# Performance work log

Hardware: AMD Instinct MI355X
Metric: run time of the kernel (lower is better)

The kernel has to match this reference:

```python
import jax, jax.numpy as jnp
import numpy as np

N_GENE = 4762
N_CELL = 847


def _graph_conv(x_src, src, dst, n_src, n_dst, W, b):
    """DGL GraphConv with norm='both': D_src^{-1/2} A D_dst^{-1/2} X W + b."""
    ones_e = jnp.ones(src.shape, jnp.float32)
    deg_out = jax.ops.segment_sum(ones_e, src, num_segments=n_src)
    norm_src = jnp.clip(deg_out, 1.0, None) ** -0.5
    feat = x_src * norm_src[:, None]            # [n_src, d]
    msg = feat[src]                              # gather  [E, d]
    agg = jax.ops.segment_sum(msg, dst, num_segments=n_dst)  # scatter-add [n_dst, d]
    deg_in = jax.ops.segment_sum(ones_e, dst, num_segments=n_dst)
    norm_dst = jnp.clip(deg_in, 1.0, None) ** -0.5
    return (agg * norm_dst[:, None]) @ W + b


def setup_inputs() -> dict:
    key = jax.random.key(0)
    ks = jax.random.split(key, 12)
    E = 200000
    d = 256
    inp = {
        "gene_emb": jax.random.normal(ks[0], (N_GENE, d), jnp.float32),
        "cell_emb": jax.random.normal(ks[1], (N_CELL, d), jnp.float32),
        "W_g2c": jax.random.normal(ks[2], (d, d), jnp.float32) * (1.0 / np.sqrt(d)),
        "b_g2c": jnp.zeros((d,), jnp.float32),
        "W_c2g": jax.random.normal(ks[3], (d, d), jnp.float32) * (1.0 / np.sqrt(d)),
        "b_c2g": jnp.zeros((d,), jnp.float32),
        "Wp": jax.random.normal(ks[4], (2 * d, 1), jnp.float32) * (1.0 / np.sqrt(2 * d)),
        "bp": jnp.zeros((1,), jnp.float32),
        "g2c_src": jax.random.randint(ks[5], (E,), 0, N_GENE, jnp.int32),
        "g2c_dst": jax.random.randint(ks[6], (E,), 0, N_CELL, jnp.int32),
        "c2g_src": jax.random.randint(ks[7], (E,), 0, N_CELL, jnp.int32),
        "c2g_dst": jax.random.randint(ks[8], (E,), 0, N_GENE, jnp.int32),
        "dec_src": jax.random.randint(ks[9], (E,), 0, N_GENE, jnp.int32),
        "dec_dst": jax.random.randint(ks[10], (E,), 0, N_CELL, jnp.int32),
    }
    return inp


def reference(gene_emb, cell_emb, W_g2c, b_g2c, W_c2g, b_c2g, Wp, bp,
              g2c_src, g2c_dst, c2g_src, c2g_dst, dec_src, dec_dst):
    # HeteroGraphConv (aggregate='sum'): each dst type receives from one relation here.
    h_cell = _graph_conv(gene_emb, g2c_src, g2c_dst, N_GENE, N_CELL, W_g2c, b_g2c)
    h_gene = _graph_conv(cell_emb, c2g_src, c2g_dst, N_CELL, N_GENE, W_c2g, b_c2g)
    h_gene = jax.nn.relu(h_gene)
    h_cell = jax.nn.relu(h_cell)
    # HeteroMLPPredictor: concat(src_h, dst_h) @ Wp + bp on dec_graph edges.
    x = jnp.concatenate([h_gene[dec_src], h_cell[dec_dst]], axis=1)  # [E_dec, 512]
    score = x @ Wp + bp                                               # [E_dec, 1]
    return (score, h_gene, h_cell)
```

## Files before the change

kernel.cpp:

```cpp
#include <hip/hip_runtime.h>

#define N_GENE 4762
#define N_CELL 847
#define NEDGE  200000
#define D      256
#define NPART  64

typedef __attribute__((ext_vector_type(8))) short short8;
typedef __attribute__((ext_vector_type(4))) float f32x4;

#define S_G_OUT 0
#define S_C_IN  (S_G_OUT + N_GENE)
#define S_C_OUT (S_C_IN + N_CELL)
#define S_G_IN  (S_C_OUT + N_CELL)
#define NBINS   (S_G_IN + N_GENE)

#define ALIGN8(x) (((x) + 7) & ~7)

#define A_DEG      0
#define A_NRM      (A_DEG + NBINS)
#define A_OFFS_C   (A_NRM + NBINS)
#define A_OFFS_G   (A_OFFS_C + N_CELL + 1)
#define A_SORT_C   ALIGN8(A_OFFS_G + N_GENE + 1)
#define A_SORT_G   (A_SORT_C + 2 * NEDGE)
#define A_PART     (A_SORT_G + 2 * NEDGE)
#define A_SG       (A_PART + NPART * NBINS)
#define A_SC       (A_SG + N_GENE)
#define A_GENE_BF  ALIGN8(A_SC + N_CELL)
#define A_CELL_BF  ALIGN8(A_GENE_BF + N_GENE * D / 2)
#define A_WT1_BF   ALIGN8(A_CELL_BF + N_CELL * D / 2)
#define A_WT2_BF   ALIGN8(A_WT1_BF + D * D / 2)
#define A_AGGC_BF  ALIGN8(A_WT2_BF + D * D / 2)
#define A_AGGG_BF  ALIGN8(A_AGGC_BF + N_CELL * D / 2)

__device__ __forceinline__ unsigned short f2bf(float f) {
    unsigned u = __float_as_uint(f);
    u = (u + 0x7FFFu + ((u >> 16) & 1u)) >> 16;
    return (unsigned short)u;
}
__device__ __forceinline__ float bf2f(unsigned short b) {
    return __uint_as_float(((unsigned)b) << 16);
}

__global__ __launch_bounds__(1024) void k_pre(
        const int* __restrict__ g2c_src, const int* __restrict__ g2c_dst,
        const int* __restrict__ c2g_src, const int* __restrict__ c2g_dst,
        const float* __restrict__ gene_emb, const float* __restrict__ cell_emb,
        const float* __restrict__ W_g2c, const float* __restrict__ W_c2g,
        int* __restrict__ partial,
        unsigned short* __restrict__ gene_bf, unsigned short* __restrict__ cell_bf,
        unsigned short* __restrict__ wt1, unsigned short* __restrict__ wt2) {
    __shared__ int sh[NBINS];
    int B = blockIdx.x, T = threadIdx.x;
    if (B < NPART) {
        for (int j = T; j < NBINS; j += 1024) sh[j] = 0;
        __syncthreads();
        const int chunk = (NEDGE + NPART - 1) / NPART;
        int e0 = B * chunk, e1 = min(NEDGE, e0 + chunk);
        for (int e = e0 + T; e < e1; e += 1024) {
            atomicAdd(&sh[S_G_OUT + g2c_src[e]], 1);
            atomicAdd(&sh[S_C_IN  + g2c_dst[e]], 1);
            atomicAdd(&sh[S_C_OUT + c2g_src[e]], 1);
            atomicAdd(&sh[S_G_IN  + c2g_dst[e]], 1);
        }
        __syncthreads();
        int* pp = partial + B * NBINS;
        for (int j = T; j < NBINS; j += 1024) pp[j] = sh[j];
    } else {
        const int NG = N_GENE * D, NC = N_CELL * D, NW = D * D;
        const int total = NG + NC + 2 * NW;
        for (int i = (B - NPART) * 1024 + T; i < total; i += NPART * 1024) {
            if (i < NG) {
                gene_bf[i] = f2bf(gene_emb[i]);
            } else if (i < NG + NC) {
                int j = i - NG;
                cell_bf[j] = f2bf(cell_emb[j]);
            } else if (i < NG + NC + NW) {
                int j = i - NG - NC;
                wt1[j] = f2bf(W_g2c[(j & 255) * D + (j >> 8)]);
            } else {
                int j = i - NG - NC - NW;
                wt2[j] = f2bf(W_c2g[(j & 255) * D + (j >> 8)]);
            }
        }
    }
}

__global__ void k_reduce(int* __restrict__ partial, int* __restrict__ deg,
                         float* __restrict__ nrm) {
    int j = blockIdx.x * blockDim.x + threadIdx.x;
    if (j < NBINS) {
        int s = 0;
        #pragma unroll
        for (int b0 = 0; b0 < NPART; b0 += 32) {
            int t[32];
            #pragma unroll
            for (int u = 0; u < 32; u++) t[u] = partial[(b0 + u) * NBINS + j];
            #pragma unroll
            for (int u = 0; u < 32; u++) { partial[(b0 + u) * NBINS + j] = s; s += t[u]; }
        }
        deg[j] = s;
        nrm[j] = rsqrtf(fmaxf((float)s, 1.0f));
    }
}

__global__ __launch_bounds__(1024) void k_scatter(
        const int* __restrict__ g2c_src, const int* __restrict__ g2c_dst,
        const int* __restrict__ c2g_src, const int* __restrict__ c2g_dst,
        const int* __restrict__ deg, const int* __restrict__ partial,
        const float* __restrict__ nrm,
        int* __restrict__ offsC, int* __restrict__ offsG,
        int2* __restrict__ sortC, int2* __restrict__ sortG) {
    __shared__ int soffs[N_GENE + 1];
    __shared__ int scur[N_GENE];
    __shared__ int wsum[16];
    int T = threadIdx.x, blk = blockIdx.x, dir = blockIdx.y;
    const int* src  = dir ? c2g_src : g2c_src;
    const int* dst  = dir ? c2g_dst : g2c_dst;
    const int* dgs  = dir ? deg + S_G_IN : deg + S_C_IN;
    const float* nsv = dir ? nrm + S_C_OUT : nrm + S_G_OUT;
    int seg         = dir ? S_G_IN : S_C_IN;
    int nb          = dir ? N_GENE : N_CELL;
    int* goffs      = dir ? offsG : offsC;
    int2* sorted    = dir ? sortG : sortC;
    int per = (nb + 1023) >> 10;
    int i0 = T * per, i1 = min(nb, i0 + per);
    int loc[5];
    int s = 0;
    for (int i = i0; i < i1; i++) { loc[i - i0] = s; s += dgs[i]; }
    int lane = T & 63, w = T >> 6;
    int t = s;
    #pragma unroll
    for (int off = 1; off < 64; off <<= 1) {
        int u = __shfl_up(t, off);
        if (lane >= off) t += u;
    }
    if (lane == 63) wsum[w] = t;
    __syncthreads();
    if (w == 0 && lane < 16) {
        int x = wsum[lane];
        #pragma unroll
        for (int off = 1; off < 16; off <<= 1) {
            int u = __shfl_up(x, off);
            if (lane >= off) x += u;
        }
        wsum[lane] = x;
    }
    __syncthreads();
    int wbase = w ? wsum[w - 1] : 0;
    int excl = wbase + t - s;
    for (int i = i0; i < i1; i++) soffs[i] = excl + loc[i - i0];
    if (T == 1023) soffs[nb] = excl + s;
    __syncthreads();
    if (blk == 0)
        for (int j = T; j <= nb; j += 1024) goffs[j] = soffs[j];
    const int* basep = partial + blk * NBINS + seg;
    for (int j = T; j < nb; j += 1024) scur[j] = soffs[j] + basep[j];
    __syncthreads();
    const int chunk = (NEDGE + NPART - 1) / NPART;
    int e0 = blk * chunk, e1 = min(NEDGE, e0 + chunk);
    for (int e = e0 + T; e < e1; e += 1024) {
        int d = dst[e], sv = src[e];
        float nv = nsv[sv];
        int pos = atomicAdd(&scur[d], 1);
        sorted[pos] = make_int2(sv, __float_as_int(nv));
    }
}

__global__ __launch_bounds__(256) void k_agg(
        const unsigned short* __restrict__ gene_bf,
        const unsigned short* __restrict__ cell_bf,
        const int2* __restrict__ sortC, const int2* __restrict__ sortG,
        const int* __restrict__ offsC, const int* __restrict__ offsG,
        const float* __restrict__ nrm,
        unsigned short* __restrict__ aggC, unsigned short* __restrict__ aggG) {
    __shared__ int    sidx[4][64];
    __shared__ float  snrm[4][64];
    __shared__ float4 pacc[4][64];
    int w = threadIdx.x >> 6, lane = threadIdx.x & 63;
    int B = blockIdx.x;
    if (B < N_CELL) {
        int d = B;
        int e0 = offsC[d], e1 = offsC[d + 1];
        int ne = e1 - e0;
        int nw = (ne + 3) >> 2;
        int a0 = e0 + w * nw, a1 = min(e1, a0 + nw);
        float ax = 0.f, ay = 0.f, az = 0.f, aw2 = 0.f;
        for (int base = a0; base < a1; base += 64) {
            int n = min(64, a1 - base);
            if (lane < n) {
                int2 pr = sortC[base + lane];
                sidx[w][lane] = pr.x;
                snrm[w][lane] = __int_as_float(pr.y);
            }
            int i = 0;
            for (; i + 4 <= n; i += 4) {
                ushort4 v0 = *(const ushort4*)&gene_bf[sidx[w][i + 0] * D + lane * 4];
                ushort4 v1 = *(const ushort4*)&gene_bf[sidx[w][i + 1] * D + lane * 4];
                ushort4 v2 = *(const ushort4*)&gene_bf[sidx[w][i + 2] * D + lane * 4];
                ushort4 v3 = *(const ushort4*)&gene_bf[sidx[w][i + 3] * D + lane * 4];
                float n0 = snrm[w][i + 0], n1 = snrm[w][i + 1];
                float n2 = snrm[w][i + 2], n3 = snrm[w][i + 3];
                ax += bf2f(v0.x)*n0 + bf2f(v1.x)*n1 + bf2f(v2.x)*n2 + bf2f(v3.x)*n3;
                ay += bf2f(v0.y)*n0 + bf2f(v1.y)*n1 + bf2f(v2.y)*n2 + bf2f(v3.y)*n3;
                az += bf2f(v0.z)*n0 + bf2f(v1.z)*n1 + bf2f(v2.z)*n2 + bf2f(v3.z)*n3;
                aw2 += bf2f(v0.w)*n0 + bf2f(v1.w)*n1 + bf2f(v2.w)*n2 + bf2f(v3.w)*n3;
            }
            for (; i < n; i++) {
                ushort4 v = *(const ushort4*)&gene_bf[sidx[w][i] * D + lane * 4];
                float nn = snrm[w][i];
                ax += bf2f(v.x)*nn; ay += bf2f(v.y)*nn;
                az += bf2f(v.z)*nn; aw2 += bf2f(v.w)*nn;
            }
        }
        pacc[w][lane] = make_float4(ax, ay, az, aw2);
        __syncthreads();
        if (w == 0) {
            float4 p0 = pacc[0][lane], p1 = pacc[1][lane];
            float4 p2 = pacc[2][lane], p3 = pacc[3][lane];
            float ndv = nrm[S_C_IN + d];
            ushort4 o;
            o.x = f2bf((p0.x + p1.x + p2.x + p3.x) * ndv);
            o.y = f2bf((p0.y + p1.y + p2.y + p3.y) * ndv);
            o.z = f2bf((p0.z + p1.z + p2.z + p3.z) * ndv);
            o.w = f2bf((p0.w + p1.w + p2.w + p3.w) * ndv);
            *(ushort4*)&aggC[d * D + lane * 4] = o;
        }
    } else {
        int g = (B - N_CELL) * 4 + w;
        if (g >= N_GENE) return;
        int e0 = offsG[g], e1 = offsG[g + 1];
        float ax = 0.f, ay = 0.f, az = 0.f, aw2 = 0.f;
        for (int base = e0; base < e1; base += 64) {
            int n = min(64, e1 - base);
            if (lane < n) {
                int2 pr = sortG[base + lane];
                sidx[w][lane] = pr.x;
                snrm[w][lane] = __int_as_float(pr.y);
            }
            int i = 0;
            for (; i + 4 <= n; i += 4) {
                ushort4 v0 = *(const ushort4*)&cell_bf[sidx[w][i + 0] * D + lane * 4];
                ushort4 v1 = *(const ushort4*)&cell_bf[sidx[w][i + 1] * D + lane * 4];
                ushort4 v2 = *(const ushort4*)&cell_bf[sidx[w][i + 2] * D + lane * 4];
                ushort4 v3 = *(const ushort4*)&cell_bf[sidx[w][i + 3] * D + lane * 4];
                float n0 = snrm[w][i + 0], n1 = snrm[w][i + 1];
                float n2 = snrm[w][i + 2], n3 = snrm[w][i + 3];
                ax += bf2f(v0.x)*n0 + bf2f(v1.x)*n1 + bf2f(v2.x)*n2 + bf2f(v3.x)*n3;
                ay += bf2f(v0.y)*n0 + bf2f(v1.y)*n1 + bf2f(v2.y)*n2 + bf2f(v3.y)*n3;
                az += bf2f(v0.z)*n0 + bf2f(v1.z)*n1 + bf2f(v2.z)*n2 + bf2f(v3.z)*n3;
                aw2 += bf2f(v0.w)*n0 + bf2f(v1.w)*n1 + bf2f(v2.w)*n2 + bf2f(v3.w)*n3;
            }
            for (; i < n; i++) {
                ushort4 v = *(const ushort4*)&cell_bf[sidx[w][i] * D + lane * 4];
                float nn = snrm[w][i];
                ax += bf2f(v.x)*nn; ay += bf2f(v.y)*nn;
                az += bf2f(v.z)*nn; aw2 += bf2f(v.w)*nn;
            }
        }
        float ndv = nrm[S_G_IN + g];
        ushort4 o;
        o.x = f2bf(ax * ndv); o.y = f2bf(ay * ndv);
        o.z = f2bf(az * ndv); o.w = f2bf(aw2 * ndv);
        *(ushort4*)&aggG[g * D + lane * 4] = o;
    }
}

__global__ __launch_bounds__(256) void k_gemm2(
        const unsigned short* __restrict__ aggC, const unsigned short* __restrict__ aggG,
        const unsigned short* __restrict__ wt1, const unsigned short* __restrict__ wt2,
        const float* __restrict__ b_g2c, const float* __restrict__ b_c2g,
        const float* __restrict__ Wp,
        float* __restrict__ hC, float* __restrict__ hG,
        float* __restrict__ sg, float* __restrict__ sc) {
    const int CT = (N_CELL + 15) / 16;
    const int GT = (N_GENE + 15) / 16;
    int wid = blockIdx.x * 4 + (threadIdx.x >> 6);
    if (wid >= CT + GT) return;
    bool isCell = wid < CT;
    int tile = isCell ? wid : wid - CT;
    int m0 = tile * 16;
    int M = isCell ? N_CELL : N_GENE;
    const unsigned short* A  = isCell ? aggC : aggG;
    const unsigned short* Wt = isCell ? wt1 : wt2;
    const float* bias = isCell ? b_g2c : b_c2g;
    const float* wp   = isCell ? Wp + D : Wp;
    float* H  = isCell ? hC : hG;
    float* sv = isCell ? sc : sg;
    int lane = threadIdx.x & 63;
    int l15 = lane & 15, quad = lane >> 4;
    int arow = m0 + l15;
    if (arow >= M) arow = M - 1;
    f32x4 acc[16];
    #pragma unroll
    for (int t = 0; t < 16; t++) acc[t] = (f32x4){0.f, 0.f, 0.f, 0.f};
    #pragma unroll
    for (int k0 = 0; k0 < D; k0 += 32) {
        short8 a = *(const short8*)&A[arow * D + k0 + quad * 8];
        #pragma unroll
        for (int t = 0; t < 16; t++) {
            short8 b = *(const short8*)&Wt[(t * 16 + l15) * D + k0 + quad * 8];
            acc[t] = __builtin_amdgcn_mfma_f32_16x16x32_bf16(a, b, acc[t], 0, 0, 0);
        }
    }
    float dot[4] = {0.f, 0.f, 0.f, 0.f};
    #pragma unroll
    for (int t = 0; t < 16; t++) {
        int col = t * 16 + l15;
        float bv = bias[col], wv = wp[col];
        #pragma unroll
        for (int r = 0; r < 4; r++) {
            int row = m0 + quad * 4 + r;
            float h = fmaxf(acc[t][r] + bv, 0.f);
            if (row < M) H[row * D + col] = h;
            dot[r] += h * wv;
        }
    }
    #pragma unroll
    for (int off = 1; off < 16; off <<= 1) {
        #pragma unroll
        for (int r = 0; r < 4; r++) dot[r] += __shfl_xor(dot[r], off);
    }
    if (l15 == 0) {
        #pragma unroll
        for (int r = 0; r < 4; r++) {
            int row = m0 + quad * 4 + r;
            if (row < M) sv[row] = dot[r];
        }
    }
}

__global__ void k_score(const int* __restrict__ dsrc, const int* __restrict__ ddst,
                        const float* __restrict__ sg, const float* __restrict__ sc,
                        const float* __restrict__ bp, float* __restrict__ out) {
    int i = blockIdx.x * blockDim.x + threadIdx.x;
    if (i < NEDGE) out[i] = sg[dsrc[i]] + sc[ddst[i]] + bp[0];
}

extern "C" void kernel_launch(void* const* d_in, const int* in_sizes, int n_in,
                              void* d_out, int out_size, void* d_ws, size_t ws_size,
                              hipStream_t stream) {
    const float* gene_emb = (const float*)d_in[0];
    const float* cell_emb = (const float*)d_in[1];
    const float* W_g2c    = (const float*)d_in[2];
    const float* b_g2c    = (const float*)d_in[3];
    const float* W_c2g    = (const float*)d_in[4];
    const float* b_c2g    = (const float*)d_in[5];
    const float* Wp       = (const float*)d_in[6];
    const float* bp       = (const float*)d_in[7];
    const int* g2c_src = (const int*)d_in[8];
    const int* g2c_dst = (const int*)d_in[9];
    const int* c2g_src = (const int*)d_in[10];
    const int* c2g_dst = (const int*)d_in[11];
    const int* dec_src = (const int*)d_in[12];
    const int* dec_dst = (const int*)d_in[13];

    int*   wsi = (int*)d_ws;
    float* wsf = (float*)d_ws;
    unsigned short* gene_bf = (unsigned short*)(wsi + A_GENE_BF);
    unsigned short* cell_bf = (unsigned short*)(wsi + A_CELL_BF);
    unsigned short* wt1     = (unsigned short*)(wsi + A_WT1_BF);
    unsigned short* wt2     = (unsigned short*)(wsi + A_WT2_BF);
    unsigned short* aggC    = (unsigned short*)(wsi + A_AGGC_BF);
    unsigned short* aggG    = (unsigned short*)(wsi + A_AGGG_BF);
    int2* sortC = (int2*)(wsi + A_SORT_C);
    int2* sortG = (int2*)(wsi + A_SORT_G);

    float* out = (float*)d_out;
    float* out_score = out;
    float* out_hgene = out + NEDGE;
    float* out_hcell = out + NEDGE + N_GENE * D;

    k_pre<<<2 * NPART, 1024, 0, stream>>>(g2c_src, g2c_dst, c2g_src, c2g_dst,
                                          gene_emb, cell_emb, W_g2c, W_c2g,
                                          wsi + A_PART, gene_bf, cell_bf, wt1, wt2);
    k_reduce<<<(NBINS + 255) / 256, 256, 0, stream>>>(wsi + A_PART, wsi + A_DEG,
                                                      wsf + A_NRM);
    {
        dim3 grid(NPART, 2);
        k_scatter<<<grid, 1024, 0, stream>>>(g2c_src, g2c_dst, c2g_src, c2g_dst,
                                             wsi + A_DEG, wsi + A_PART, wsf + A_NRM,
                                             wsi + A_OFFS_C, wsi + A_OFFS_G,
                                             sortC, sortG);
    }
    k_agg<<<N_CELL + (N_GENE + 3) / 4, 256, 0, stream>>>(
        gene_bf, cell_bf, sortC, sortG, wsi + A_OFFS_C, wsi + A_OFFS_G,
        wsf + A_NRM, aggC, aggG);
    {
        const int CT = (N_CELL + 15) / 16, GT = (N_GENE + 15) / 16;
        k_gemm2<<<(CT + GT + 3) / 4, 256, 0, stream>>>(aggC, aggG, wt1, wt2,
                                                       b_g2c, b_c2g, Wp,
                                                       out_hcell, out_hgene,
                                                       wsf + A_SG, wsf + A_SC);
    }
    k_score<<<(NEDGE + 255) / 256, 256, 0, stream>>>(dec_src, dec_dst,
                                                     wsf + A_SG, wsf + A_SC, bp, out_score);
}
```

Measured before the change: 162.4 us.

## Fuse neighbor aggregation into the MFMA GEMM via a shared-memory tile

Merges the separate aggregation and GEMM kernels into one kernel. Each block gathers and normalizes 16 destination rows into an LDS bf16 tile, then runs the 16x256 MFMA GEMM, with each wave producing 4 column tiles. The per-row score partials are reduced across waves in shared memory. This drops the intermediate agg buffers, their global round trip and one launch. In exchange, each wave now aggregates 4 whole rows serially instead of splitting one cell's edges across waves, so high-degree cell rows become a long serial path across only about 350 blocks.

```diff
diff --git a/kernel.cpp b/kernel.cpp
--- a/kernel.cpp
+++ b/kernel.cpp
@@ -30,8 +30,8 @@
 #define A_CELL_BF  ALIGN8(A_GENE_BF + N_GENE * D / 2)
 #define A_WT1_BF   ALIGN8(A_CELL_BF + N_CELL * D / 2)
 #define A_WT2_BF   ALIGN8(A_WT1_BF + D * D / 2)
-#define A_AGGC_BF  ALIGN8(A_WT2_BF + D * D / 2)
-#define A_AGGG_BF  ALIGN8(A_AGGC_BF + N_CELL * D / 2)
+
+#define TPITCH 264
 
 __device__ __forceinline__ unsigned short f2bf(float f) {
     unsigned u = __float_as_uint(f);
@@ -167,151 +167,104 @@
     }
 }
 
-__global__ __launch_bounds__(256) void k_agg(
+__global__ __launch_bounds__(256) void k_aggemm(
         const unsigned short* __restrict__ gene_bf,
         const unsigned short* __restrict__ cell_bf,
+        const unsigned short* __restrict__ wt1, const unsigned short* __restrict__ wt2,
         const int2* __restrict__ sortC, const int2* __restrict__ sortG,
         const int* __restrict__ offsC, const int* __restrict__ offsG,
         const float* __restrict__ nrm,
-        unsigned short* __restrict__ aggC, unsigned short* __restrict__ aggG) {
-    __shared__ int    sidx[4][64];
-    __shared__ float  snrm[4][64];
-    __shared__ float4 pacc[4][64];
-    int w = threadIdx.x >> 6, lane = threadIdx.x & 63;
-    int B = blockIdx.x;
-    if (B < N_CELL) {
-        int d = B;
-        int e0 = offsC[d], e1 = offsC[d + 1];
-        int ne = e1 - e0;
-        int nw = (ne + 3) >> 2;
-        int a0 = e0 + w * nw, a1 = min(e1, a0 + nw);
-        float ax = 0.f, ay = 0.f, az = 0.f, aw2 = 0.f;
-        for (int base = a0; base < a1; base += 64) {
-            int n = min(64, a1 - base);
-            if (lane < n) {
-                int2 pr = sortC[base + lane];
-                sidx[w][lane] = pr.x;
-                snrm[w][lane] = __int_as_float(pr.y);
-            }
-            int i = 0;
-            for (; i + 4 <= n; i += 4) {
-                ushort4 v0 = *(const ushort4*)&gene_bf[sidx[w][i + 0] * D + lane * 4];
-                ushort4 v1 = *(const ushort4*)&gene_bf[sidx[w][i + 1] * D + lane * 4];
-                ushort4 v2 = *(const ushort4*)&gene_bf[sidx[w][i + 2] * D + lane * 4];
-                ushort4 v3 = *(const ushort4*)&gene_bf[sidx[w][i + 3] * D + lane * 4];
-                float n0 = snrm[w][i + 0], n1 = snrm[w][i + 1];
-                float n2 = snrm[w][i + 2], n3 = snrm[w][i + 3];
-                ax += bf2f(v0.x)*n0 + bf2f(v1.x)*n1 + bf2f(v2.x)*n2 + bf2f(v3.x)*n3;
-                ay += bf2f(v0.y)*n0 + bf2f(v1.y)*n1 + bf2f(v2.y)*n2 + bf2f(v3.y)*n3;
-                az += bf2f(v0.z)*n0 + bf2f(v1.z)*n1 + bf2f(v2.z)*n2 + bf2f(v3.z)*n3;
-                aw2 += bf2f(v0.w)*n0 + bf2f(v1.w)*n1 + bf2f(v2.w)*n2 + bf2f(v3.w)*n3;
-            }
-            for (; i < n; i++) {
-                ushort4 v = *(const ushort4*)&gene_bf[sidx[w][i] * D + lane * 4];
-                float nn = snrm[w][i];
-                ax += bf2f(v.x)*nn; ay += bf2f(v.y)*nn;
-                az += bf2f(v.z)*nn; aw2 += bf2f(v.w)*nn;
-            }
-        }
-        pacc[w][lane] = make_float4(ax, ay, az, aw2);
-        __syncthreads();
-        if (w == 0) {
-            float4 p0 = pacc[0][lane], p1 = pacc[1][lane];
-            float4 p2 = pacc[2][lane], p3 = pacc[3][lane];
-            float ndv = nrm[S_C_IN + d];
-            ushort4 o;
-            o.x = f2bf((p0.x + p1.x + p2.x + p3.x) * ndv);
-            o.y = f2bf((p0.y + p1.y + p2.y + p3.y) * ndv);
-            o.z = f2bf((p0.z + p1.z + p2.z + p3.z) * ndv);
-            o.w = f2bf((p0.w + p1.w + p2.w + p3.w) * ndv);
-            *(ushort4*)&aggC[d * D + lane * 4] = o;
-        }
-    } else {
-        int g = (B - N_CELL) * 4 + w;
-        if (g >= N_GENE) return;
-        int e0 = offsG[g], e1 = offsG[g + 1];
-        float ax = 0.f, ay = 0.f, az = 0.f, aw2 = 0.f;
-        for (int base = e0; base < e1; base += 64) {
-            int n = min(64, e1 - base);
-            if (lane < n) {
-                int2 pr = sortG[base + lane];
-                sidx[w][lane] = pr.x;
-                snrm[w][lane] = __int_as_float(pr.y);
-            }
-            int i = 0;
-            for (; i + 4 <= n; i += 4) {
-                ushort4 v0 = *(const ushort4*)&cell_bf[sidx[w][i + 0] * D + lane * 4];
-                ushort4 v1 = *(const ushort4*)&cell_bf[sidx[w][i + 1] * D + lane * 4];
-                ushort4 v2 = *(const ushort4*)&cell_bf[sidx[w][i + 2] * D + lane * 4];
-                ushort4 v3 = *(const ushort4*)&cell_bf[sidx[w][i + 3] * D + lane * 4];
-                float n0 = snrm[w][i + 0], n1 = snrm[w][i + 1];
-                float n2 = snrm[w][i + 2], n3 = snrm[w][i + 3];
-                ax += bf2f(v0.x)*n0 + bf2f(v1.x)*n1 + bf2f(v2.x)*n2 + bf2f(v3.x)*n3;
-                ay += bf2f(v0.y)*n0 + bf2f(v1.y)*n1 + bf2f(v2.y)*n2 + bf2f(v3.y)*n3;
-                az += bf2f(v0.z)*n0 + bf2f(v1.z)*n1 + bf2f(v2.z)*n2 + bf2f(v3.z)*n3;
-                aw2 += bf2f(v0.w)*n0 + bf2f(v1.w)*n1 + bf2f(v2.w)*n2 + bf2f(v3.w)*n3;
-            }
-            for (; i < n; i++) {
-                ushort4 v = *(const ushort4*)&cell_bf[sidx[w][i] * D + lane * 4];
-                float nn = snrm[w][i];
-                ax += bf2f(v.x)*nn; ay += bf2f(v.y)*nn;
-                az += bf2f(v.z)*nn; aw2 += bf2f(v.w)*nn;
-            }
-        }
-        float ndv = nrm[S_G_IN + g];
-        ushort4 o;
-        o.x = f2bf(ax * ndv); o.y = f2bf(ay * ndv);
-        o.z = f2bf(az * ndv); o.w = f2bf(aw2 * ndv);
-        *(ushort4*)&aggG[g * D + lane * 4] = o;
-    }
-}
-
-__global__ __launch_bounds__(256) void k_gemm2(
-        const unsigned short* __restrict__ aggC, const unsigned short* __restrict__ aggG,
-        const unsigned short* __restrict__ wt1, const unsigned short* __restrict__ wt2,
         const float* __restrict__ b_g2c, const float* __restrict__ b_c2g,
         const float* __restrict__ Wp,
         float* __restrict__ hC, float* __restrict__ hG,
         float* __restrict__ sg, float* __restrict__ sc) {
     const int CT = (N_CELL + 15) / 16;
-    const int GT = (N_GENE + 15) / 16;
-    int wid = blockIdx.x * 4 + (threadIdx.x >> 6);
-    if (wid >= CT + GT) return;
-    bool isCell = wid < CT;
-    int tile = isCell ? wid : wid - CT;
-    int m0 = tile * 16;
+    __shared__ int            sidx[4][64];
+    __shared__ float          snrm[4][64];
+    __shared__ unsigned short tile[16][TPITCH];
+    __shared__ float          pdot[4][16];
+    int B = blockIdx.x;
+    int w = threadIdx.x >> 6, lane = threadIdx.x & 63;
+    bool isCell = B < CT;
+    int tidx = isCell ? B : B - CT;
+    int m0 = tidx * 16;
     int M = isCell ? N_CELL : N_GENE;
-    const unsigned short* A  = isCell ? aggC : aggG;
-    const unsigned short* Wt = isCell ? wt1 : wt2;
-    const float* bias = isCell ? b_g2c : b_c2g;
-    const float* wp   = isCell ? Wp + D : Wp;
+    const unsigned short* emb = isCell ? gene_bf : cell_bf;
+    const int2* sorted        = isCell ? sortC : sortG;
+    const int*  offs          = isCell ? offsC : offsG;
+    const float* ndvp         = isCell ? nrm + S_C_IN : nrm + S_G_IN;
+    const unsigned short* Wt  = isCell ? wt1 : wt2;
+    const float* bias         = isCell ? b_g2c : b_c2g;
+    const float* wp           = isCell ? Wp + D : Wp;
     float* H  = isCell ? hC : hG;
     float* sv = isCell ? sc : sg;
-    int lane = threadIdx.x & 63;
+
+    #pragma unroll
+    for (int j = 0; j < 4; j++) {
+        int row = w * 4 + j;
+        int node = m0 + row;
+        ushort4 o = make_ushort4(0, 0, 0, 0);
+        if (node < M) {
+            int e0 = offs[node], e1 = offs[node + 1];
+            float ax = 0.f, ay = 0.f, az = 0.f, aw2 = 0.f;
+            for (int base = e0; base < e1; base += 64) {
+                int n = min(64, e1 - base);
+                if (lane < n) {
+                    int2 pr = sorted[base + lane];
+                    sidx[w][lane] = pr.x;
+                    snrm[w][lane] = __int_as_float(pr.y);
+                }
+                int i = 0;
+                for (; i + 4 <= n; i += 4) {
+                    ushort4 v0 = *(const ushort4*)&emb[sidx[w][i + 0] * D + lane * 4];
+                    ushort4 v1 = *(const ushort4*)&emb[sidx[w][i + 1] * D + lane * 4];
+                    ushort4 v2 = *(const ushort4*)&emb[sidx[w][i + 2] * D + lane * 4];
+                    ushort4 v3 = *(const ushort4*)&emb[sidx[w][i + 3] * D + lane * 4];
+                    float n0 = snrm[w][i + 0], n1 = snrm[w][i + 1];
+                    float n2 = snrm[w][i + 2], n3 = snrm[w][i + 3];
+                    ax += bf2f(v0.x)*n0 + bf2f(v1.x)*n1 + bf2f(v2.x)*n2 + bf2f(v3.x)*n3;
+                    ay += bf2f(v0.y)*n0 + bf2f(v1.y)*n1 + bf2f(v2.y)*n2 + bf2f(v3.y)*n3;
+                    az += bf2f(v0.z)*n0 + bf2f(v1.z)*n1 + bf2f(v2.z)*n2 + bf2f(v3.z)*n3;
+                    aw2 += bf2f(v0.w)*n0 + bf2f(v1.w)*n1 + bf2f(v2.w)*n2 + bf2f(v3.w)*n3;
+                }
+                for (; i < n; i++) {
+                    ushort4 v = *(const ushort4*)&emb[sidx[w][i] * D + lane * 4];
+                    float nn = snrm[w][i];
+                    ax += bf2f(v.x)*nn; ay += bf2f(v.y)*nn;
+                    az += bf2f(v.z)*nn; aw2 += bf2f(v.w)*nn;
+                }
+            }
+            float ndv = ndvp[node];
+            o.x = f2bf(ax * ndv); o.y = f2bf(ay * ndv);
+            o.z = f2bf(az * ndv); o.w = f2bf(aw2 * ndv);
+        }
+        *(ushort4*)&tile[row][lane * 4] = o;
+    }
+    __syncthreads();
+
     int l15 = lane & 15, quad = lane >> 4;
-    int arow = m0 + l15;
-    if (arow >= M) arow = M - 1;
-    f32x4 acc[16];
-    #pragma unroll
-    for (int t = 0; t < 16; t++) acc[t] = (f32x4){0.f, 0.f, 0.f, 0.f};
+    f32x4 acc[4];
+    #pragma unroll
+    for (int i = 0; i < 4; i++) acc[i] = (f32x4){0.f, 0.f, 0.f, 0.f};
     #pragma unroll
     for (int k0 = 0; k0 < D; k0 += 32) {
-        short8 a = *(const short8*)&A[arow * D + k0 + quad * 8];
-        #pragma unroll
-        for (int t = 0; t < 16; t++) {
-            short8 b = *(const short8*)&Wt[(t * 16 + l15) * D + k0 + quad * 8];
-            acc[t] = __builtin_amdgcn_mfma_f32_16x16x32_bf16(a, b, acc[t], 0, 0, 0);
+        short8 a = *(const short8*)&tile[l15][k0 + quad * 8];
+        #pragma unroll
+        for (int i = 0; i < 4; i++) {
+            int ct = w * 4 + i;
+            short8 b = *(const short8*)&Wt[(ct * 16 + l15) * D + k0 + quad * 8];
+            acc[i] = __builtin_amdgcn_mfma_f32_16x16x32_bf16(a, b, acc[i], 0, 0, 0);
         }
     }
     float dot[4] = {0.f, 0.f, 0.f, 0.f};
     #pragma unroll
-    for (int t = 0; t < 16; t++) {
-        int col = t * 16 + l15;
+    for (int i = 0; i < 4; i++) {
+        int col = (w * 4 + i) * 16 + l15;
         float bv = bias[col], wv = wp[col];
         #pragma unroll
         for (int r = 0; r < 4; r++) {
             int row = m0 + quad * 4 + r;
-            float h = fmaxf(acc[t][r] + bv, 0.f);
+            float h = fmaxf(acc[i][r] + bv, 0.f);
             if (row < M) H[row * D + col] = h;
             dot[r] += h * wv;
         }
@@ -323,9 +276,15 @@
     }
     if (l15 == 0) {
         #pragma unroll
-        for (int r = 0; r < 4; r++) {
-            int row = m0 + quad * 4 + r;
-            if (row < M) sv[row] = dot[r];
+        for (int r = 0; r < 4; r++) pdot[w][quad * 4 + r] = dot[r];
+    }
+    __syncthreads();
+    if (threadIdx.x < 16) {
+        int row = m0 + threadIdx.x;
+        if (row < M) {
+            float s2 = pdot[0][threadIdx.x] + pdot[1][threadIdx.x] +
+                       pdot[2][threadIdx.x] + pdot[3][threadIdx.x];
+            sv[row] = s2;
         }
     }
 }
@@ -361,8 +320,6 @@
     unsigned short* cell_bf = (unsigned short*)(wsi + A_CELL_BF);
     unsigned short* wt1     = (unsigned short*)(wsi + A_WT1_BF);
     unsigned short* wt2     = (unsigned short*)(wsi + A_WT2_BF);
-    unsigned short* aggC    = (unsigned short*)(wsi + A_AGGC_BF);
-    unsigned short* aggG    = (unsigned short*)(wsi + A_AGGG_BF);
     int2* sortC = (int2*)(wsi + A_SORT_C);
     int2* sortG = (int2*)(wsi + A_SORT_G);
 
@@ -383,15 +340,14 @@
                                              wsi + A_OFFS_C, wsi + A_OFFS_G,
                                              sortC, sortG);
     }
-    k_agg<<<N_CELL + (N_GENE + 3) / 4, 256, 0, stream>>>(
-        gene_bf, cell_bf, sortC, sortG, wsi + A_OFFS_C, wsi + A_OFFS_G,
-        wsf + A_NRM, aggC, aggG);
     {
         const int CT = (N_CELL + 15) / 16, GT = (N_GENE + 15) / 16;
-        k_gemm2<<<(CT + GT + 3) / 4, 256, 0, stream>>>(aggC, aggG, wt1, wt2,
-                                                       b_g2c, b_c2g, Wp,
-                                                       out_hcell, out_hgene,
-                                                       wsf + A_SG, wsf + A_SC);
+        k_aggemm<<<CT + GT, 256, 0, stream>>>(gene_bf, cell_bf, wt1, wt2,
+                                              sortC, sortG,
+                                              wsi + A_OFFS_C, wsi + A_OFFS_G,
+                                              wsf + A_NRM, b_g2c, b_c2g, Wp,
+                                              out_hcell, out_hgene,
+                                              wsf + A_SG, wsf + A_SC);
     }
     k_score<<<(NEDGE + 255) / 256, 256, 0, stream>>>(dec_src, dec_dst,
                                                      wsf + A_SG, wsf + A_SC, bp, out_score);
```

Result: slower. 204.6 us (+26.0%).
